# Kernel tuning notes

Hardware: AMD Instinct MI355X
Metric: run time of the kernel (lower is better)

Reference implementation:

```python
import jax, jax.numpy as jnp
import numpy as np

B, H, HKV, D = 64, 32, 8, 128          # batch(seqs), q heads, kv heads, head dim
PAGE, PAGES_PER_SEQ, NUM_PAGES = 32, 64, 4096
SMAX = PAGES_PER_SEQ * PAGE            # 2048 max context tokens
SCALE = 0.08838834764831843            # 1/sqrt(head_dim)


def setup_inputs() -> dict:
    key = jax.random.key(0)
    ks = jax.random.split(key, 8)
    q = jax.random.normal(ks[0], (B, H, D), jnp.float32)
    k = jax.random.normal(ks[1], (B, HKV, D), jnp.float32)
    v = jax.random.normal(ks[2], (B, HKV, D), jnp.float32)
    k_cache = jax.random.normal(ks[3], (NUM_PAGES, PAGE, HKV, D), jnp.float32)
    v_cache = jax.random.normal(ks[4], (NUM_PAGES, PAGE, HKV, D), jnp.float32)
    block_tables = jax.random.randint(ks[5], (B, PAGES_PER_SEQ), 0, NUM_PAGES, jnp.int32)
    context_lens = jax.random.randint(ks[6], (B,), 1, SMAX + 1, jnp.int32)
    slot_mapping = jax.random.randint(ks[7], (B,), 0, NUM_PAGES * PAGE, jnp.int32)
    return {"q": q, "k": k, "v": v, "k_cache": k_cache, "v_cache": v_cache,
            "block_tables": block_tables, "context_lens": context_lens,
            "slot_mapping": slot_mapping}


def reference(q, k, v, k_cache, v_cache, block_tables, context_lens, slot_mapping):
    # --- store_kvcache: scatter new per-token k/v into flat slot space ---
    kc = k_cache.reshape(-1, HKV, D).at[slot_mapping].set(k)
    vc = v_cache.reshape(-1, HKV, D).at[slot_mapping].set(v)
    kc = kc.reshape(NUM_PAGES, PAGE, HKV, D)
    vc = vc.reshape(NUM_PAGES, PAGE, HKV, D)

    # --- paged decode: gather pages per sequence via block tables ---
    gk = kc[block_tables].reshape(B, SMAX, HKV, D)  # [B, S, HKV, D]
    gv = vc[block_tables].reshape(B, SMAX, HKV, D)

    # --- GQA attention: group q heads over kv heads (repeat_interleave) ---
    G = H // HKV
    qg = q.reshape(B, HKV, G, D)
    scores = jnp.einsum('bkgd,bskd->bkgs', qg, gk) * SCALE  # [B, HKV, G, S]
    valid = jnp.arange(SMAX)[None, :] < context_lens[:, None]  # [B, S]
    scores = jnp.where(valid[:, None, None, :], scores, -jnp.inf)
    p = jax.nn.softmax(scores, axis=-1)
    out = jnp.einsum('bkgs,bskd->bkgd', p, gv).reshape(B, H, D)
    return out
```

## Files before the change

kernel.cpp:

```cpp
#include <hip/hip_runtime.h>

#define NB 64
#define NH 32
#define NKV 8
#define HD 128
#define NG 4
#define PAGE 32
#define PPS 64
#define SMAX 2048
#define CHUNK 128
#define CPP (CHUNK / PAGE)
#define NCH (SMAX / CHUNK)
#define SCALE 0.08838834764831843f

template <int CTRL>
__device__ __forceinline__ float dpp_xadd(float v) {
    int t = __builtin_amdgcn_update_dpp(0, __float_as_int(v), CTRL, 0xF, 0xF, false);
    return v + __int_as_float(t);
}

__device__ __forceinline__ float rsum32(float x) {
    x = dpp_xadd<0xB1>(x);
    x = dpp_xadd<0x4E>(x);
    x = dpp_xadd<0x124>(x);
    x = dpp_xadd<0x128>(x);
    int y = __builtin_amdgcn_ds_swizzle(__float_as_int(x), 0x401F);
    return x + __int_as_float(y);
}

__device__ __forceinline__ void oupd(
    float d0, float d1, float d2, float d3, const float4 vv,
    float& m0, float& m1, float& m2, float& m3,
    float& l0, float& l1, float& l2, float& l3,
    float4& a0, float4& a1, float4& a2, float4& a3)
{
    if (d0 > m0 || d1 > m1 || d2 > m2 || d3 > m3) {
        const float n0 = fmaxf(m0, d0), n1 = fmaxf(m1, d1);
        const float n2 = fmaxf(m2, d2), n3 = fmaxf(m3, d3);
        const float e0 = __expf(m0 - n0), e1 = __expf(m1 - n1);
        const float e2 = __expf(m2 - n2), e3 = __expf(m3 - n3);
        const float p0 = __expf(d0 - n0), p1 = __expf(d1 - n1);
        const float p2 = __expf(d2 - n2), p3 = __expf(d3 - n3);
        m0 = n0; m1 = n1; m2 = n2; m3 = n3;
        l0 = l0 * e0 + p0; l1 = l1 * e1 + p1;
        l2 = l2 * e2 + p2; l3 = l3 * e3 + p3;
        a0.x = a0.x * e0 + p0 * vv.x; a0.y = a0.y * e0 + p0 * vv.y;
        a0.z = a0.z * e0 + p0 * vv.z; a0.w = a0.w * e0 + p0 * vv.w;
        a1.x = a1.x * e1 + p1 * vv.x; a1.y = a1.y * e1 + p1 * vv.y;
        a1.z = a1.z * e1 + p1 * vv.z; a1.w = a1.w * e1 + p1 * vv.w;
        a2.x = a2.x * e2 + p2 * vv.x; a2.y = a2.y * e2 + p2 * vv.y;
        a2.z = a2.z * e2 + p2 * vv.z; a2.w = a2.w * e2 + p2 * vv.w;
        a3.x = a3.x * e3 + p3 * vv.x; a3.y = a3.y * e3 + p3 * vv.y;
        a3.z = a3.z * e3 + p3 * vv.z; a3.w = a3.w * e3 + p3 * vv.w;
    } else {
        const float p0 = __expf(d0 - m0), p1 = __expf(d1 - m1);
        const float p2 = __expf(d2 - m2), p3 = __expf(d3 - m3);
        l0 += p0; l1 += p1; l2 += p2; l3 += p3;
        a0.x += p0 * vv.x; a0.y += p0 * vv.y; a0.z += p0 * vv.z; a0.w += p0 * vv.w;
        a1.x += p1 * vv.x; a1.y += p1 * vv.y; a1.z += p1 * vv.z; a1.w += p1 * vv.w;
        a2.x += p2 * vv.x; a2.y += p2 * vv.y; a2.z += p2 * vv.z; a2.w += p2 * vv.w;
        a3.x += p3 * vv.x; a3.y += p3 * vv.y; a3.z += p3 * vv.z; a3.w += p3 * vv.w;
    }
}

__global__ __launch_bounds__(256) void paged_attn_split(
    const float* __restrict__ q,
    const float* __restrict__ knew,
    const float* __restrict__ vnew,
    const float* __restrict__ kcache,
    const float* __restrict__ vcache,
    const int*  __restrict__ btab,
    const int*  __restrict__ ctxlen,
    const int*  __restrict__ slotmap,
    float* __restrict__ pacc,
    float* __restrict__ pml)
{
    const int kh  = blockIdx.x;
    const int b   = blockIdx.y;
    const int c   = blockIdx.z;
    const int tid = threadIdx.x;

    const int S  = ctxlen[b];
    const int c0 = c * CHUNK;
    if (c0 >= S) return;
    const int send = min(S, c0 + CHUNK);

    __shared__ int   bt_s[CPP];
    __shared__ int   ovr_s[CHUNK];
    __shared__ float acc_s[8][NG][HD];
    __shared__ float ml_s[8][NG][2];

    if (tid < CPP) bt_s[tid] = btab[b * PPS + c * CPP + tid];
    if (tid < CHUNK) ovr_s[tid] = -1;
    __syncthreads();
    if (tid < NB) {
        const int slot = slotmap[tid];
        const int pg = slot >> 5, pos = slot & 31;
        #pragma unroll
        for (int i = 0; i < CPP; ++i)
            if (bt_s[i] == pg) atomicMax(&ovr_s[i * PAGE + pos], tid);
    }
    __syncthreads();

    const int hw = tid >> 5;
    const int ln = tid & 31;

    const float* qb = q + ((size_t)(b * NH + kh * NG)) * HD + 4 * ln;
    const float4 q0 = *(const float4*)(qb + 0 * HD);
    const float4 q1 = *(const float4*)(qb + 1 * HD);
    const float4 q2 = *(const float4*)(qb + 2 * HD);
    const float4 q3 = *(const float4*)(qb + 3 * HD);

    float m0 = -INFINITY, m1 = -INFINITY, m2 = -INFINITY, m3 = -INFINITY;
    float l0 = 0.f, l1 = 0.f, l2 = 0.f, l3 = 0.f;
    float4 a0 = {0,0,0,0}, a1 = {0,0,0,0}, a2 = {0,0,0,0}, a3 = {0,0,0,0};

    auto addr = [&](int sg, const float*& kp, const float*& vp) {
        const int r  = sg - c0;
        const int ov = ovr_s[r];
        if (ov >= 0) {
            const size_t o = ((size_t)ov * NKV + kh) * HD + 4 * ln;
            kp = knew + o; vp = vnew + o;
        } else {
            const size_t o = (((size_t)bt_s[r >> 5] * PAGE + (r & 31)) * NKV + kh) * HD + 4 * ln;
            kp = kcache + o; vp = vcache + o;
        }
    };

    int s = c0 + hw;
    for (; s + 8 < send; s += 16) {
        const float *kpA, *vpA, *kpB, *vpB;
        addr(s,     kpA, vpA);
        addr(s + 8, kpB, vpB);
        const float4 kA = *(const float4*)kpA;
        const float4 kB = *(const float4*)kpB;
        const float4 vA = *(const float4*)vpA;
        const float4 vB = *(const float4*)vpB;

        float dA0 = q0.x*kA.x + q0.y*kA.y + q0.z*kA.z + q0.w*kA.w;
        float dA1 = q1.x*kA.x + q1.y*kA.y + q1.z*kA.z + q1.w*kA.w;
        float dA2 = q2.x*kA.x + q2.y*kA.y + q2.z*kA.z + q2.w*kA.w;
        float dA3 = q3.x*kA.x + q3.y*kA.y + q3.z*kA.z + q3.w*kA.w;
        float dB0 = q0.x*kB.x + q0.y*kB.y + q0.z*kB.z + q0.w*kB.w;
        float dB1 = q1.x*kB.x + q1.y*kB.y + q1.z*kB.z + q1.w*kB.w;
        float dB2 = q2.x*kB.x + q2.y*kB.y + q2.z*kB.z + q2.w*kB.w;
        float dB3 = q3.x*kB.x + q3.y*kB.y + q3.z*kB.z + q3.w*kB.w;

        dA0 = rsum32(dA0) * SCALE; dA1 = rsum32(dA1) * SCALE;
        dA2 = rsum32(dA2) * SCALE; dA3 = rsum32(dA3) * SCALE;
        dB0 = rsum32(dB0) * SCALE; dB1 = rsum32(dB1) * SCALE;
        dB2 = rsum32(dB2) * SCALE; dB3 = rsum32(dB3) * SCALE;

        oupd(dA0, dA1, dA2, dA3, vA, m0,m1,m2,m3, l0,l1,l2,l3, a0,a1,a2,a3);
        oupd(dB0, dB1, dB2, dB3, vB, m0,m1,m2,m3, l0,l1,l2,l3, a0,a1,a2,a3);
    }
    if (s < send) {
        const float *kp, *vp;
        addr(s, kp, vp);
        const float4 kv = *(const float4*)kp;
        const float4 vv = *(const float4*)vp;
        float d0 = q0.x*kv.x + q0.y*kv.y + q0.z*kv.z + q0.w*kv.w;
        float d1 = q1.x*kv.x + q1.y*kv.y + q1.z*kv.z + q1.w*kv.w;
        float d2 = q2.x*kv.x + q2.y*kv.y + q2.z*kv.z + q2.w*kv.w;
        float d3 = q3.x*kv.x + q3.y*kv.y + q3.z*kv.z + q3.w*kv.w;
        d0 = rsum32(d0) * SCALE; d1 = rsum32(d1) * SCALE;
        d2 = rsum32(d2) * SCALE; d3 = rsum32(d3) * SCALE;
        oupd(d0, d1, d2, d3, vv, m0,m1,m2,m3, l0,l1,l2,l3, a0,a1,a2,a3);
    }

    *(float4*)&acc_s[hw][0][4 * ln] = a0;
    *(float4*)&acc_s[hw][1][4 * ln] = a1;
    *(float4*)&acc_s[hw][2][4 * ln] = a2;
    *(float4*)&acc_s[hw][3][4 * ln] = a3;
    if (ln == 0) {
        ml_s[hw][0][0] = m0; ml_s[hw][0][1] = l0;
        ml_s[hw][1][0] = m1; ml_s[hw][1][1] = l1;
        ml_s[hw][2][0] = m2; ml_s[hw][2][1] = l2;
        ml_s[hw][3][0] = m3; ml_s[hw][3][1] = l3;
    }
    __syncthreads();

    for (int o = tid; o < NG * HD; o += 256) {
        const int h = o >> 7;
        const int d = o & 127;
        float M = -INFINITY;
        #pragma unroll
        for (int w = 0; w < 8; ++w) M = fmaxf(M, ml_s[w][h][0]);
        float L = 0.f, val = 0.f;
        #pragma unroll
        for (int w = 0; w < 8; ++w) {
            const float mm = ml_s[w][h][0];
            const float sc = (mm == -INFINITY) ? 0.f : __expf(mm - M);
            L   += sc * ml_s[w][h][1];
            val += sc * acc_s[w][h][d];
        }
        const size_t idx = ((size_t)((b * NKV + kh) * NCH + c) * NG + h);
        pacc[idx * HD + d] = val;
        if (d == 0) { pml[idx * 2] = M; pml[idx * 2 + 1] = L; }
    }
}

__global__ __launch_bounds__(256) void paged_attn_combine(
    const int*  __restrict__ ctxlen,
    const float* __restrict__ pacc,
    const float* __restrict__ pml,
    float* __restrict__ out)
{
    const int kh  = blockIdx.x;
    const int b   = blockIdx.y;
    const int tid = threadIdx.x;
    const int S   = ctxlen[b];
    const int nch = (S + CHUNK - 1) / CHUNK;

    __shared__ float ml_s[NCH][NG][2];
    if (tid < nch * NG) {
        const int cc = tid / NG, h = tid % NG;
        const size_t idx = ((size_t)((b * NKV + kh) * NCH + cc) * NG + h);
        ml_s[cc][h][0] = pml[idx * 2];
        ml_s[cc][h][1] = pml[idx * 2 + 1];
    }
    __syncthreads();

    for (int o = tid; o < NG * HD; o += 256) {
        const int h = o >> 7;
        const int d = o & 127;
        float M = -INFINITY;
        for (int cc = 0; cc < nch; ++cc) M = fmaxf(M, ml_s[cc][h][0]);
        float L = 0.f, val = 0.f;
        for (int cc = 0; cc < nch; ++cc) {
            const float sc = __expf(ml_s[cc][h][0] - M);
            L   += sc * ml_s[cc][h][1];
            val += sc * pacc[((size_t)((b * NKV + kh) * NCH + cc) * NG + h) * HD + d];
        }
        out[((size_t)(b * NH + kh * NG + h)) * HD + d] = val / L;
    }
}

__global__ __launch_bounds__(256) void paged_attn_mono(
    const float* __restrict__ q, const float* __restrict__ knew,
    const float* __restrict__ vnew, const float* __restrict__ kcache,
    const float* __restrict__ vcache, const int* __restrict__ btab,
    const int* __restrict__ ctxlen, const int* __restrict__ slotmap,
    float* __restrict__ out)
{
    const int kh  = blockIdx.x;
    const int b   = blockIdx.y;
    const int tid = threadIdx.x;

    __shared__ int   bt_s[PPS];
    __shared__ int   slot_s[NB];
    __shared__ short ovr_s[SMAX];
    __shared__ float acc_s[8][NG][HD];
    __shared__ float ml_s[8][NG][2];

    if (tid < PPS)              bt_s[tid]        = btab[b * PPS + tid];
    if (tid >= 64 && tid < 128) slot_s[tid - 64] = slotmap[tid - 64];
    for (int i = tid; i < SMAX; i += 256) ovr_s[i] = -1;
    __syncthreads();
    if (tid < PPS) {
        const int page = bt_s[tid];
        for (int j = 0; j < NB; ++j) {
            const int slot = slot_s[j];
            if ((slot >> 5) == page) ovr_s[tid * PAGE + (slot & 31)] = (short)j;
        }
    }
    __syncthreads();

    const int S  = ctxlen[b];
    const int hw = tid >> 5;
    const int ln = tid & 31;

    const float* qb = q + ((size_t)(b * NH + kh * NG)) * HD + 4 * ln;
    const float4 q0 = *(const float4*)(qb + 0 * HD);
    const float4 q1 = *(const float4*)(qb + 1 * HD);
    const float4 q2 = *(const float4*)(qb + 2 * HD);
    const float4 q3 = *(const float4*)(qb + 3 * HD);

    float m0 = -INFINITY, m1 = -INFINITY, m2 = -INFINITY, m3 = -INFINITY;
    float l0 = 0.f, l1 = 0.f, l2 = 0.f, l3 = 0.f;
    float4 a0 = {0,0,0,0}, a1 = {0,0,0,0}, a2 = {0,0,0,0}, a3 = {0,0,0,0};

    for (int s = hw; s < S; s += 8) {
        const int ov = ovr_s[s];
        const float* kp; const float* vp;
        if (ov >= 0) {
            const size_t o = ((size_t)ov * NKV + kh) * HD + 4 * ln;
            kp = knew + o; vp = vnew + o;
        } else {
            const size_t o = (((size_t)bt_s[s >> 5] * PAGE + (s & 31)) * NKV + kh) * HD + 4 * ln;
            kp = kcache + o; vp = vcache + o;
        }
        const float4 kv = *(const float4*)kp;
        const float4 vv = *(const float4*)vp;
        float d0 = q0.x*kv.x + q0.y*kv.y + q0.z*kv.z + q0.w*kv.w;
        float d1 = q1.x*kv.x + q1.y*kv.y + q1.z*kv.z + q1.w*kv.w;
        float d2 = q2.x*kv.x + q2.y*kv.y + q2.z*kv.z + q2.w*kv.w;
        float d3 = q3.x*kv.x + q3.y*kv.y + q3.z*kv.z + q3.w*kv.w;
        d0 = rsum32(d0) * SCALE; d1 = rsum32(d1) * SCALE;
        d2 = rsum32(d2) * SCALE; d3 = rsum32(d3) * SCALE;
        oupd(d0, d1, d2, d3, vv, m0,m1,m2,m3, l0,l1,l2,l3, a0,a1,a2,a3);
    }

    *(float4*)&acc_s[hw][0][4 * ln] = a0;
    *(float4*)&acc_s[hw][1][4 * ln] = a1;
    *(float4*)&acc_s[hw][2][4 * ln] = a2;
    *(float4*)&acc_s[hw][3][4 * ln] = a3;
    if (ln == 0) {
        ml_s[hw][0][0] = m0; ml_s[hw][0][1] = l0;
        ml_s[hw][1][0] = m1; ml_s[hw][1][1] = l1;
        ml_s[hw][2][0] = m2; ml_s[hw][2][1] = l2;
        ml_s[hw][3][0] = m3; ml_s[hw][3][1] = l3;
    }
    __syncthreads();
    for (int o = tid; o < NG * HD; o += 256) {
        const int h = o >> 7, d = o & 127;
        float M = -INFINITY;
        #pragma unroll
        for (int w = 0; w < 8; ++w) M = fmaxf(M, ml_s[w][h][0]);
        float L = 0.f, val = 0.f;
        #pragma unroll
        for (int w = 0; w < 8; ++w) {
            const float mm = ml_s[w][h][0];
            const float sc = (mm == -INFINITY) ? 0.f : __expf(mm - M);
            L += sc * ml_s[w][h][1];
            val += sc * acc_s[w][h][d];
        }
        out[((size_t)(b * NH + kh * NG + h)) * HD + d] = val / L;
    }
}

extern "C" void kernel_launch(void* const* d_in, const int* in_sizes, int n_in,
                              void* d_out, int out_size, void* d_ws, size_t ws_size,
                              hipStream_t stream) {
    const float* q  = (const float*)d_in[0];
    const float* k  = (const float*)d_in[1];
    const float* v  = (const float*)d_in[2];
    const float* kc = (const float*)d_in[3];
    const float* vc = (const float*)d_in[4];
    const int* bt   = (const int*)d_in[5];
    const int* cl   = (const int*)d_in[6];
    const int* sm   = (const int*)d_in[7];
    float* out = (float*)d_out;

    const size_t nidx = (size_t)NB * NKV * NCH * NG;
    const size_t need = nidx * (HD + 2) * sizeof(float);

    if (ws_size >= need) {
        float* pacc = (float*)d_ws;
        float* pml  = pacc + nidx * HD;
        dim3 gs(NKV, NB, NCH);
        paged_attn_split<<<gs, 256, 0, stream>>>(q, k, v, kc, vc, bt, cl, sm, pacc, pml);
        dim3 gc(NKV, NB);
        paged_attn_combine<<<gc, 256, 0, stream>>>(cl, pacc, pml, out);
    } else {
        dim3 g(NKV, NB);
        paged_attn_mono<<<g, 256, 0, stream>>>(q, k, v, kc, vc, bt, cl, sm, out);
    }
}
```

Before: 106.7 us.

## Map warps to KV heads per chunk and halve split chunk size

The split kernel now launches one block per (batch, chunk) rather than per (kv head, batch, chunk). Each of its 8 half-wave groups handles one KV head and walks every token of the chunk, so the token-row loads for all heads of a token are spread across warps. With this mapping the in-block shared-memory reduction and its barrier go away, and each warp writes its partial (m, l, acc) straight to the workspace. The chunk size drops from 128 to 64, which doubles the number of partial chunks the combine kernel has to merge. Each warp now works through a longer serial chain of tokens, so there is less latency hiding per warp.

```diff
diff --git a/kernel.cpp b/kernel.cpp
--- a/kernel.cpp
+++ b/kernel.cpp
@@ -8,7 +8,7 @@
 #define PAGE 32
 #define PPS 64
 #define SMAX 2048
-#define CHUNK 128
+#define CHUNK 64
 #define CPP (CHUNK / PAGE)
 #define NCH (SMAX / CHUNK)
 #define SCALE 0.08838834764831843f
@@ -75,22 +75,19 @@
     float* __restrict__ pacc,
     float* __restrict__ pml)
 {
-    const int kh  = blockIdx.x;
-    const int b   = blockIdx.y;
-    const int c   = blockIdx.z;
+    const int b   = blockIdx.x;
+    const int c   = blockIdx.y;
     const int tid = threadIdx.x;
 
     const int S  = ctxlen[b];
     const int c0 = c * CHUNK;
     if (c0 >= S) return;
-    const int send = min(S, c0 + CHUNK);
-
-    __shared__ int   bt_s[CPP];
-    __shared__ int   ovr_s[CHUNK];
-    __shared__ float acc_s[8][NG][HD];
-    __shared__ float ml_s[8][NG][2];
-
-    if (tid < CPP) bt_s[tid] = btab[b * PPS + c * CPP + tid];
+    const int nt = min(S - c0, CHUNK);
+
+    __shared__ int bt_s[CPP];
+    __shared__ int ovr_s[CHUNK];
+
+    if (tid < CPP)   bt_s[tid]  = btab[b * PPS + c * CPP + tid];
     if (tid < CHUNK) ovr_s[tid] = -1;
     __syncthreads();
     if (tid < NB) {
@@ -105,7 +102,7 @@
     const int hw = tid >> 5;
     const int ln = tid & 31;
 
-    const float* qb = q + ((size_t)(b * NH + kh * NG)) * HD + 4 * ln;
+    const float* qb = q + ((size_t)(b * NH + hw * NG)) * HD + 4 * ln;
     const float4 q0 = *(const float4*)(qb + 0 * HD);
     const float4 q1 = *(const float4*)(qb + 1 * HD);
     const float4 q2 = *(const float4*)(qb + 2 * HD);
@@ -115,23 +112,22 @@
     float l0 = 0.f, l1 = 0.f, l2 = 0.f, l3 = 0.f;
     float4 a0 = {0,0,0,0}, a1 = {0,0,0,0}, a2 = {0,0,0,0}, a3 = {0,0,0,0};
 
-    auto addr = [&](int sg, const float*& kp, const float*& vp) {
-        const int r  = sg - c0;
+    auto addr = [&](int r, const float*& kp, const float*& vp) {
         const int ov = ovr_s[r];
         if (ov >= 0) {
-            const size_t o = ((size_t)ov * NKV + kh) * HD + 4 * ln;
+            const size_t o = ((size_t)ov * NKV + hw) * HD + 4 * ln;
             kp = knew + o; vp = vnew + o;
         } else {
-            const size_t o = (((size_t)bt_s[r >> 5] * PAGE + (r & 31)) * NKV + kh) * HD + 4 * ln;
+            const size_t o = (((size_t)bt_s[r >> 5] * PAGE + (r & 31)) * NKV + hw) * HD + 4 * ln;
             kp = kcache + o; vp = vcache + o;
         }
     };
 
-    int s = c0 + hw;
-    for (; s + 8 < send; s += 16) {
+    int r = 0;
+    for (; r + 1 < nt; r += 2) {
         const float *kpA, *vpA, *kpB, *vpB;
-        addr(s,     kpA, vpA);
-        addr(s + 8, kpB, vpB);
+        addr(r,     kpA, vpA);
+        addr(r + 1, kpB, vpB);
         const float4 kA = *(const float4*)kpA;
         const float4 kB = *(const float4*)kpB;
         const float4 vA = *(const float4*)vpA;
@@ -154,9 +150,9 @@
         oupd(dA0, dA1, dA2, dA3, vA, m0,m1,m2,m3, l0,l1,l2,l3, a0,a1,a2,a3);
         oupd(dB0, dB1, dB2, dB3, vB, m0,m1,m2,m3, l0,l1,l2,l3, a0,a1,a2,a3);
     }
-    if (s < send) {
+    if (r < nt) {
         const float *kp, *vp;
-        addr(s, kp, vp);
+        addr(r, kp, vp);
         const float4 kv = *(const float4*)kp;
         const float4 vv = *(const float4*)vp;
         float d0 = q0.x*kv.x + q0.y*kv.y + q0.z*kv.z + q0.w*kv.w;
@@ -168,35 +164,16 @@
         oupd(d0, d1, d2, d3, vv, m0,m1,m2,m3, l0,l1,l2,l3, a0,a1,a2,a3);
     }
 
-    *(float4*)&acc_s[hw][0][4 * ln] = a0;
-    *(float4*)&acc_s[hw][1][4 * ln] = a1;
-    *(float4*)&acc_s[hw][2][4 * ln] = a2;
-    *(float4*)&acc_s[hw][3][4 * ln] = a3;
+    const size_t idx0 = ((size_t)(b * NKV + hw) * NCH + c) * NG;
+    *(float4*)&pacc[(idx0 + 0) * HD + 4 * ln] = a0;
+    *(float4*)&pacc[(idx0 + 1) * HD + 4 * ln] = a1;
+    *(float4*)&pacc[(idx0 + 2) * HD + 4 * ln] = a2;
+    *(float4*)&pacc[(idx0 + 3) * HD + 4 * ln] = a3;
     if (ln == 0) {
-        ml_s[hw][0][0] = m0; ml_s[hw][0][1] = l0;
-        ml_s[hw][1][0] = m1; ml_s[hw][1][1] = l1;
-        ml_s[hw][2][0] = m2; ml_s[hw][2][1] = l2;
-        ml_s[hw][3][0] = m3; ml_s[hw][3][1] = l3;
-    }
-    __syncthreads();
-
-    for (int o = tid; o < NG * HD; o += 256) {
-        const int h = o >> 7;
-        const int d = o & 127;
-        float M = -INFINITY;
-        #pragma unroll
-        for (int w = 0; w < 8; ++w) M = fmaxf(M, ml_s[w][h][0]);
-        float L = 0.f, val = 0.f;
-        #pragma unroll
-        for (int w = 0; w < 8; ++w) {
-            const float mm = ml_s[w][h][0];
-            const float sc = (mm == -INFINITY) ? 0.f : __expf(mm - M);
-            L   += sc * ml_s[w][h][1];
-            val += sc * acc_s[w][h][d];
-        }
-        const size_t idx = ((size_t)((b * NKV + kh) * NCH + c) * NG + h);
-        pacc[idx * HD + d] = val;
-        if (d == 0) { pml[idx * 2] = M; pml[idx * 2 + 1] = L; }
+        pml[(idx0 + 0) * 2] = m0; pml[(idx0 + 0) * 2 + 1] = l0;
+        pml[(idx0 + 1) * 2] = m1; pml[(idx0 + 1) * 2 + 1] = l1;
+        pml[(idx0 + 2) * 2] = m2; pml[(idx0 + 2) * 2 + 1] = l2;
+        pml[(idx0 + 3) * 2] = m3; pml[(idx0 + 3) * 2 + 1] = l3;
     }
 }
 
@@ -348,7 +325,7 @@
     if (ws_size >= need) {
         float* pacc = (float*)d_ws;
         float* pml  = pacc + nidx * HD;
-        dim3 gs(NKV, NB, NCH);
+        dim3 gs(NB, NCH);
         paged_attn_split<<<gs, 256, 0, stream>>>(q, k, v, kc, vc, bt, cl, sm, pacc, pml);
         dim3 gc(NKV, NB);
         paged_attn_combine<<<gc, 256, 0, stream>>>(cl, pacc, pml, out);
```

Result: slower. 134.7 us (+26.2%).
